# Performance work log

Measured on AMD Instinct MI355X. Metric: run time of the kernel, lower is better.

The kernel has to match this reference:

```python
import jax, jax.numpy as jnp
import numpy as np
from math import sqrt

HEADS = 16
D_MODEL = 1024
HEAD_DIM = D_MODEL // HEADS  # 64
B, SEQ = 2, 2048


def setup_inputs() -> dict:
    key = jax.random.key(0)
    ks = jax.random.split(key, 8)
    k = jax.random.normal(ks[0], (B, SEQ, D_MODEL), dtype=jnp.float32)
    q = jax.random.normal(ks[1], (B, SEQ, D_MODEL), dtype=jnp.float32)
    v = jax.random.normal(ks[2], (B, SEQ, D_MODEL), dtype=jnp.float32)
    # causal mask, broadcast over batch and heads; masked_fill where mask == 0
    mask = jnp.tril(jnp.ones((SEQ, SEQ), dtype=jnp.int32))[None, None, :, :]
    s = 1.0 / sqrt(HEAD_DIM)
    Wq = jax.random.normal(ks[3], (HEAD_DIM, HEAD_DIM), dtype=jnp.float32) * s
    Wk = jax.random.normal(ks[4], (HEAD_DIM, HEAD_DIM), dtype=jnp.float32) * s
    Wv = jax.random.normal(ks[5], (HEAD_DIM, HEAD_DIM), dtype=jnp.float32) * s
    Wo = jax.random.normal(ks[6], (D_MODEL, D_MODEL), dtype=jnp.float32) * (1.0 / sqrt(D_MODEL))
    bo = jax.random.normal(ks[7], (D_MODEL,), dtype=jnp.float32) * 0.01
    return {"key": k, "query": q, "value": v, "mask": mask,
            "Wq": Wq, "Wk": Wk, "Wv": Wv, "Wo": Wo, "bo": bo}


def reference(key, query, value, mask, Wq, Wk, Wv, Wo, bo):
    b, q_len, d = query.shape
    k_len = key.shape[1]
    hd = d // HEADS
    # reshape to [b, len, heads, head_dim]
    k = key.reshape(b, k_len, HEADS, hd)
    q = query.reshape(b, q_len, HEADS, hd)
    v = value.reshape(b, k_len, HEADS, hd)
    # per-head-dim Linear (weights shared across heads); torch Linear: y = x @ W.T
    k = jnp.einsum('bkhd,ed->bkhe', k, Wk)
    q = jnp.einsum('bqhd,ed->bqhe', q, Wq)
    v = jnp.einsum('bvhd,ed->bvhe', v, Wv)
    # full attention matrix [b, h, q, k]
    product = jnp.einsum('bqhd,bkhd->bhqk', q, k)
    # NOTE: original masks BEFORE scaling by 1/sqrt(head_dim)
    product = jnp.where(mask == 0, jnp.float32(-1e20), product)
    product = product / jnp.float32(sqrt(hd))
    score = jax.nn.softmax(product, axis=-1)
    out = jnp.einsum('bhqv,bvhd->bqhd', score, v).reshape(b, q_len, d)
    out = out @ Wo.T + bo
    return out
```

## Files before the change

### kernel.cpp

```cpp
#include <hip/hip_runtime.h>

typedef __bf16 bf16x8 __attribute__((ext_vector_type(8)));
typedef float  f32x4  __attribute__((ext_vector_type(4)));
typedef unsigned int uint32x4 __attribute__((ext_vector_type(4)));

#define MFMA16(a, b, c) __builtin_amdgcn_mfma_f32_16x16x32_bf16((a), (b), (c), 0, 0, 0)

constexpr int SEQ = 2048;
constexpr int DM  = 1024;
constexpr int NH  = 16;
constexpr int HD  = 64;
constexpr int BATCH = 2;


__device__ inline bf16x8 ld8_f32(const float* p) {
    f32x4 a = *(const f32x4*)p;
    f32x4 b = *(const f32x4*)(p + 4);
    bf16x8 r;
    r[0] = (__bf16)a[0]; r[1] = (__bf16)a[1]; r[2] = (__bf16)a[2]; r[3] = (__bf16)a[3];
    r[4] = (__bf16)b[0]; r[5] = (__bf16)b[1]; r[6] = (__bf16)b[2]; r[7] = (__bf16)b[3];
    return r;
}

__global__ __launch_bounds__(256)
void proj_kernel(const float* __restrict__ Xq, const float* __restrict__ Xk,
                 const float* __restrict__ Xv,
                 const float* __restrict__ Wq, const float* __restrict__ Wk,
                 const float* __restrict__ Wv,
                 __bf16* __restrict__ Qp, __bf16* __restrict__ Kp,
                 __bf16* __restrict__ Vp)
{
    const int tid  = threadIdx.x;
    const int w    = tid >> 6;
    const int lane = tid & 63;
    const int quad = lane >> 4;
    const int l16  = lane & 15;
    const int sblk = blockIdx.x;
    const int bh   = blockIdx.y;
    const int tz   = blockIdx.z;

    const float* X = (tz == 0) ? Xq : (tz == 1) ? Xk : Xv;
    const float* W = (tz == 0) ? Wq : (tz == 1) ? Wk : Wv;
    __bf16*      O = (tz == 0) ? Qp : (tz == 1) ? Kp : Vp;
    const float scale = (tz == 0) ? (0.125f * 1.44269504088896f) : 1.0f;

    const int b = bh >> 4, h = bh & 15;
    const int mrow = sblk * 64 + w * 16 + l16;

    const size_t xoff = (size_t)(b * SEQ + mrow) * DM + h * HD + quad * 8;
    bf16x8 a0 = ld8_f32(X + xoff);
    bf16x8 a1 = ld8_f32(X + xoff + 32);

    f32x4 acc[4];
    #pragma unroll
    for (int nt = 0; nt < 4; ++nt) {
        const size_t woff = (size_t)(nt * 16 + l16) * HD + quad * 8;
        bf16x8 b0 = ld8_f32(W + woff);
        bf16x8 b1 = ld8_f32(W + woff + 32);
        f32x4 c = {0.f, 0.f, 0.f, 0.f};
        c = MFMA16(a0, b0, c);
        c = MFMA16(a1, b1, c);
        acc[nt] = c;
    }

    __bf16* obase = O + (size_t)bh * SEQ * HD;
    #pragma unroll
    for (int nt = 0; nt < 4; ++nt) {
        #pragma unroll
        for (int r = 0; r < 4; ++r) {
            const int srow = sblk * 64 + w * 16 + quad * 4 + r;
            obase[(size_t)srow * HD + nt * 16 + l16] = (__bf16)(acc[nt][r] * scale);
        }
    }
}

__global__ __launch_bounds__(256, 2)
void attn_kernel(const __bf16* __restrict__ Qp, const __bf16* __restrict__ Kp,
                 const __bf16* __restrict__ Vp, __bf16* __restrict__ AO)
{
    __shared__ __align__(16) unsigned int K_lds[2][64 * 36];
    __shared__ __align__(16) unsigned int VT2[2][64 * 36];
    __shared__ __align__(16) __bf16 P_lds[4][16 * 72];

    const int tid  = threadIdx.x;
    const int w    = tid >> 6;
    const int lane = tid & 63;
    const int quad = lane >> 4;
    const int l16  = lane & 15;
    const int pr   = blockIdx.x;
    const int bh   = blockIdx.y;

    const __bf16* Qb = Qp + (size_t)bh * SEQ * HD;
    const __bf16* Kb = Kp + (size_t)bh * SEQ * HD;
    const __bf16* Vb = Vp + (size_t)bh * SEQ * HD;

    bf16x8 onesf;
    #pragma unroll
    for (int i = 0; i < 8; ++i) onesf[i] = (l16 == 0) ? (__bf16)1.0f : (__bf16)0.0f;

    const int krow = tid >> 3, kcol = tid & 7;
    const int jp = tid & 31, d0 = (tid >> 5) * 8;

    #pragma unroll
    for (int phase = 0; phase < 2; ++phase) {
        const int tile = (phase == 0) ? (31 - pr) : pr;
        const int q0   = tile * 64;
        const int nkc  = tile + 1;

        __syncthreads();

        const int mrow = q0 + w * 16 + l16;
        bf16x8 qa0 = *(const bf16x8*)(Qb + (size_t)mrow * HD + quad * 8);
        bf16x8 qa1 = *(const bf16x8*)(Qb + (size_t)mrow * HD + quad * 8 + 32);

        f32x4 accO[4];
        #pragma unroll
        for (int nt = 0; nt < 4; ++nt) { f32x4 z = {0.f,0.f,0.f,0.f}; accO[nt] = z; }
        f32x4 acc5 = {0.f, 0.f, 0.f, 0.f};

        uint32x4 kpre0 = *(const uint32x4*)(Kb + (size_t)krow * HD + kcol * 8);
        uint32x4 kpre1 = *(const uint32x4*)(Kb + (size_t)(krow + 32) * HD + kcol * 8);
        uint32x4 vlo   = *(const uint32x4*)(Vb + (size_t)(2 * jp) * HD + d0);
        uint32x4 vhi   = *(const uint32x4*)(Vb + (size_t)(2 * jp + 1) * HD + d0);

        for (int kc = 0; kc < nkc; ++kc) {
            const int buf = kc & 1;
            *(uint32x4*)&K_lds[buf][krow * 36 + kcol * 4]        = kpre0;
            *(uint32x4*)&K_lds[buf][(krow + 32) * 36 + kcol * 4] = kpre1;
            #pragma unroll
            for (int i2 = 0; i2 < 4; ++i2) {
                const unsigned int va = vlo[i2], vb = vhi[i2];
                VT2[buf][(d0 + 2 * i2    ) * 36 + jp] = (va & 0xffffu) | (vb << 16);
                VT2[buf][(d0 + 2 * i2 + 1) * 36 + jp] = (va >> 16) | (vb & 0xffff0000u);
            }
            __syncthreads();

            if (kc + 1 < nkc) {
                const size_t o = (size_t)(kc + 1) * 64;
                kpre0 = *(const uint32x4*)(Kb + (o + krow) * HD + kcol * 8);
                kpre1 = *(const uint32x4*)(Kb + (o + krow + 32) * HD + kcol * 8);
                vlo   = *(const uint32x4*)(Vb + (o + 2 * jp) * HD + d0);
                vhi   = *(const uint32x4*)(Vb + (o + 2 * jp + 1) * HD + d0);
            }

            f32x4 s[4];
            #pragma unroll
            for (int nt = 0; nt < 4; ++nt) {
                const unsigned int* kb = &K_lds[buf][(nt * 16 + l16) * 36 + quad * 4];
                bf16x8 kb0 = *(const bf16x8*)(kb);
                bf16x8 kb1 = *(const bf16x8*)(kb + 16);
                f32x4 c = {0.f, 0.f, 0.f, 0.f};
                c = MFMA16(qa0, kb0, c);
                c = MFMA16(qa1, kb1, c);
                s[nt] = c;
            }
            if (kc == tile) {
                #pragma unroll
                for (int nt = 0; nt < 4; ++nt) {
                    const int j = kc * 64 + nt * 16 + l16;
                    #pragma unroll
                    for (int r = 0; r < 4; ++r) {
                        const int qrow = q0 + w * 16 + quad * 4 + r;
                        if (j > qrow) s[nt][r] = -1e30f;
                    }
                }
            }
            #pragma unroll
            for (int nt = 0; nt < 4; ++nt) {
                #pragma unroll
                for (int r = 0; r < 4; ++r) {
                    P_lds[w][(quad * 4 + r) * 72 + nt * 16 + l16] =
                        (__bf16)exp2f(s[nt][r]);
                }
            }
            asm volatile("" ::: "memory");
            bf16x8 pa0 = *(const bf16x8*)&P_lds[w][l16 * 72 + quad * 8];
            bf16x8 pa1 = *(const bf16x8*)&P_lds[w][l16 * 72 + quad * 8 + 32];
            #pragma unroll
            for (int nt = 0; nt < 4; ++nt) {
                const unsigned int* vb2 = &VT2[buf][(nt * 16 + l16) * 36 + quad * 4];
                bf16x8 vb0 = *(const bf16x8*)(vb2);
                bf16x8 vb1 = *(const bf16x8*)(vb2 + 16);
                accO[nt] = MFMA16(pa0, vb0, accO[nt]);
                accO[nt] = MFMA16(pa1, vb1, accO[nt]);
            }
            acc5 = MFMA16(pa0, onesf, acc5);
            acc5 = MFMA16(pa1, onesf, acc5);
        }

        const int b = bh >> 4, h = bh & 15;
        float inv[4];
        #pragma unroll
        for (int r = 0; r < 4; ++r) {
            const float ls = __shfl(acc5[r], quad * 16, 64);
            inv[r] = 1.0f / ls;
        }
        #pragma unroll
        for (int nt = 0; nt < 4; ++nt) {
            #pragma unroll
            for (int r = 0; r < 4; ++r) {
                const int qrow = q0 + w * 16 + quad * 4 + r;
                AO[(size_t)(b * SEQ + qrow) * DM + h * HD + nt * 16 + l16] =
                    (__bf16)(accO[nt][r] * inv[r]);
            }
        }
    }
}

__global__ __launch_bounds__(256)
void wconv_kernel(const float* __restrict__ Wo, __bf16* __restrict__ Wb)
{
    const size_t i = ((size_t)blockIdx.x * 256 + threadIdx.x) * 8;
    *(bf16x8*)(Wb + i) = ld8_f32(Wo + i);
}

__global__ __launch_bounds__(256)
void ogemm_kernel(const __bf16* __restrict__ AO, const __bf16* __restrict__ Wb,
                  const float* __restrict__ bo, float* __restrict__ out)
{
    __shared__ __align__(16) unsigned int A_lds[2][64 * 36];
    __shared__ __align__(16) unsigned int B_lds[2][128 * 36];

    const int tid  = threadIdx.x;
    const int w    = tid >> 6;
    const int lane = tid & 63;
    const int quad = lane >> 4;
    const int l16  = lane & 15;
    const int m0   = blockIdx.x * 64;
    const int n0   = blockIdx.y * 128;

    const int row = tid >> 3, c = tid & 7;

    f32x4 acc[8];
    #pragma unroll
    for (int nt = 0; nt < 8; ++nt) { f32x4 z = {0.f,0.f,0.f,0.f}; acc[nt] = z; }

    uint32x4 apre[2], bpre[4];
    #pragma unroll
    for (int i = 0; i < 2; ++i)
        apre[i] = *(const uint32x4*)(AO + (size_t)(m0 + row + i * 32) * DM + c * 8);
    #pragma unroll
    for (int i = 0; i < 4; ++i)
        bpre[i] = *(const uint32x4*)(Wb + (size_t)(n0 + row + i * 32) * DM + c * 8);

    for (int kc = 0; kc < DM / 64; ++kc) {
        const int buf = kc & 1;
        #pragma unroll
        for (int i = 0; i < 2; ++i)
            *(uint32x4*)&A_lds[buf][(row + i * 32) * 36 + c * 4] = apre[i];
        #pragma unroll
        for (int i = 0; i < 4; ++i)
            *(uint32x4*)&B_lds[buf][(row + i * 32) * 36 + c * 4] = bpre[i];
        __syncthreads();

        if (kc + 1 < DM / 64) {
            const size_t o = (size_t)(kc + 1) * 64;
            #pragma unroll
            for (int i = 0; i < 2; ++i)
                apre[i] = *(const uint32x4*)(AO + (size_t)(m0 + row + i * 32) * DM + o + c * 8);
            #pragma unroll
            for (int i = 0; i < 4; ++i)
                bpre[i] = *(const uint32x4*)(Wb + (size_t)(n0 + row + i * 32) * DM + o + c * 8);
        }

        #pragma unroll
        for (int ks = 0; ks < 2; ++ks) {
            bf16x8 a = *(const bf16x8*)&A_lds[buf][(w * 16 + l16) * 36 + ks * 16 + quad * 4];
            #pragma unroll
            for (int nt = 0; nt < 8; ++nt) {
                bf16x8 bb = *(const bf16x8*)&B_lds[buf][(nt * 16 + l16) * 36 + ks * 16 + quad * 4];
                acc[nt] = MFMA16(a, bb, acc[nt]);
            }
        }
    }

    #pragma unroll
    for (int nt = 0; nt < 8; ++nt) {
        const int n = n0 + nt * 16 + l16;
        const float bof = bo[n];
        #pragma unroll
        for (int r = 0; r < 4; ++r) {
            const int m = m0 + w * 16 + quad * 4 + r;
            out[(size_t)m * DM + n] = acc[nt][r] + bof;
        }
    }
}

extern "C" void kernel_launch(void* const* d_in, const int* in_sizes, int n_in,
                              void* d_out, int out_size, void* d_ws, size_t ws_size,
                              hipStream_t stream)
{
    const float* key   = (const float*)d_in[0];
    const float* query = (const float*)d_in[1];
    const float* value = (const float*)d_in[2];
    const float* Wq = (const float*)d_in[4];
    const float* Wk = (const float*)d_in[5];
    const float* Wv = (const float*)d_in[6];
    const float* Wo = (const float*)d_in[7];
    const float* bo = (const float*)d_in[8];

    const size_t per = (size_t)BATCH * NH * SEQ * HD;
    __bf16* Qp = (__bf16*)d_ws;
    __bf16* Kp = Qp + per;
    __bf16* Vp = Kp + per;
    __bf16* AO = Vp + per;
    __bf16* Wb = Kp;

    proj_kernel<<<dim3(SEQ / 64, BATCH * NH, 3), 256, 0, stream>>>(
        query, key, value, Wq, Wk, Wv, Qp, Kp, Vp);
    attn_kernel<<<dim3(SEQ / 128, BATCH * NH), 256, 0, stream>>>(Qp, Kp, Vp, AO);
    wconv_kernel<<<dim3(DM * DM / (256 * 8)), 256, 0, stream>>>(Wo, Wb);
    ogemm_kernel<<<dim3(BATCH * SEQ / 64, DM / 128), 256, 0, stream>>>(
        AO, Wb, bo, (float*)d_out);
}
```

Before: 198.7 us.

## Keep softmax probabilities in registers via transposed S and 16x16x16 MFMA for PV

Result: no change. 200.1 us (+0.7%).

```diff
diff --git a/kernel.cpp b/kernel.cpp
--- a/kernel.cpp
+++ b/kernel.cpp
@@ -3,8 +3,10 @@
 typedef __bf16 bf16x8 __attribute__((ext_vector_type(8)));
 typedef float  f32x4  __attribute__((ext_vector_type(4)));
 typedef unsigned int uint32x4 __attribute__((ext_vector_type(4)));
-
-#define MFMA16(a, b, c) __builtin_amdgcn_mfma_f32_16x16x32_bf16((a), (b), (c), 0, 0, 0)
+typedef short  s16x4  __attribute__((ext_vector_type(4)));
+
+#define MFMA16(a, b, c)  __builtin_amdgcn_mfma_f32_16x16x32_bf16((a), (b), (c), 0, 0, 0)
+#define MFMAK16(a, b, c) __builtin_amdgcn_mfma_f32_16x16x16bf16_1k((a), (b), (c), 0, 0, 0)
 
 constexpr int SEQ = 2048;
 constexpr int DM  = 1024;
@@ -12,6 +14,8 @@
 constexpr int HD  = 64;
 constexpr int BATCH = 2;
 
+
+union Bf4 { __bf16 h[4]; s16x4 v; unsigned int u[2]; };
 
 __device__ inline bf16x8 ld8_f32(const float* p) {
     f32x4 a = *(const f32x4*)p;
@@ -80,7 +84,6 @@
 {
     __shared__ __align__(16) unsigned int K_lds[2][64 * 36];
     __shared__ __align__(16) unsigned int VT2[2][64 * 36];
-    __shared__ __align__(16) __bf16 P_lds[4][16 * 72];
 
     const int tid  = threadIdx.x;
     const int w    = tid >> 6;
@@ -94,9 +97,9 @@
     const __bf16* Kb = Kp + (size_t)bh * SEQ * HD;
     const __bf16* Vb = Vp + (size_t)bh * SEQ * HD;
 
-    bf16x8 onesf;
-    #pragma unroll
-    for (int i = 0; i < 8; ++i) onesf[i] = (l16 == 0) ? (__bf16)1.0f : (__bf16)0.0f;
+    Bf4 ones_a;
+    #pragma unroll
+    for (int i = 0; i < 4; ++i) ones_a.h[i] = (l16 == 0) ? (__bf16)1.0f : (__bf16)0.0f;
 
     const int krow = tid >> 3, kcol = tid & 7;
     const int jp = tid & 31, d0 = (tid >> 5) * 8;
@@ -109,13 +112,13 @@
 
         __syncthreads();
 
-        const int mrow = q0 + w * 16 + l16;
-        bf16x8 qa0 = *(const bf16x8*)(Qb + (size_t)mrow * HD + quad * 8);
-        bf16x8 qa1 = *(const bf16x8*)(Qb + (size_t)mrow * HD + quad * 8 + 32);
-
-        f32x4 accO[4];
-        #pragma unroll
-        for (int nt = 0; nt < 4; ++nt) { f32x4 z = {0.f,0.f,0.f,0.f}; accO[nt] = z; }
+        const int qrow = q0 + w * 16 + l16;
+        bf16x8 qa0 = *(const bf16x8*)(Qb + (size_t)qrow * HD + quad * 8);
+        bf16x8 qa1 = *(const bf16x8*)(Qb + (size_t)qrow * HD + quad * 8 + 32);
+
+        f32x4 accT[4];
+        #pragma unroll
+        for (int dm = 0; dm < 4; ++dm) { f32x4 z = {0.f,0.f,0.f,0.f}; accT[dm] = z; }
         f32x4 acc5 = {0.f, 0.f, 0.f, 0.f};
 
         uint32x4 kpre0 = *(const uint32x4*)(Kb + (size_t)krow * HD + kcol * 8);
@@ -143,66 +146,57 @@
                 vhi   = *(const uint32x4*)(Vb + (o + 2 * jp + 1) * HD + d0);
             }
 
-            f32x4 s[4];
+            f32x4 st[4];
             #pragma unroll
             for (int nt = 0; nt < 4; ++nt) {
                 const unsigned int* kb = &K_lds[buf][(nt * 16 + l16) * 36 + quad * 4];
                 bf16x8 kb0 = *(const bf16x8*)(kb);
                 bf16x8 kb1 = *(const bf16x8*)(kb + 16);
                 f32x4 c = {0.f, 0.f, 0.f, 0.f};
-                c = MFMA16(qa0, kb0, c);
-                c = MFMA16(qa1, kb1, c);
-                s[nt] = c;
+                c = MFMA16(kb0, qa0, c);
+                c = MFMA16(kb1, qa1, c);
+                st[nt] = c;
             }
             if (kc == tile) {
                 #pragma unroll
                 for (int nt = 0; nt < 4; ++nt) {
-                    const int j = kc * 64 + nt * 16 + l16;
                     #pragma unroll
                     for (int r = 0; r < 4; ++r) {
-                        const int qrow = q0 + w * 16 + quad * 4 + r;
-                        if (j > qrow) s[nt][r] = -1e30f;
+                        const int j = kc * 64 + nt * 16 + quad * 4 + r;
+                        if (j > qrow) st[nt][r] = -1e30f;
                     }
                 }
             }
+            Bf4 pf[4];
             #pragma unroll
             for (int nt = 0; nt < 4; ++nt) {
                 #pragma unroll
-                for (int r = 0; r < 4; ++r) {
-                    P_lds[w][(quad * 4 + r) * 72 + nt * 16 + l16] =
-                        (__bf16)exp2f(s[nt][r]);
+                for (int r = 0; r < 4; ++r) pf[nt].h[r] = (__bf16)exp2f(st[nt][r]);
+            }
+            #pragma unroll
+            for (int nt = 0; nt < 4; ++nt) {
+                #pragma unroll
+                for (int dm = 0; dm < 4; ++dm) {
+                    Bf4 va;
+                    va.u[0] = VT2[buf][(dm * 16 + l16) * 36 + nt * 8 + quad * 2];
+                    va.u[1] = VT2[buf][(dm * 16 + l16) * 36 + nt * 8 + quad * 2 + 1];
+                    accT[dm] = MFMAK16(va.v, pf[nt].v, accT[dm]);
                 }
-            }
-            asm volatile("" ::: "memory");
-            bf16x8 pa0 = *(const bf16x8*)&P_lds[w][l16 * 72 + quad * 8];
-            bf16x8 pa1 = *(const bf16x8*)&P_lds[w][l16 * 72 + quad * 8 + 32];
-            #pragma unroll
-            for (int nt = 0; nt < 4; ++nt) {
-                const unsigned int* vb2 = &VT2[buf][(nt * 16 + l16) * 36 + quad * 4];
-                bf16x8 vb0 = *(const bf16x8*)(vb2);
-                bf16x8 vb1 = *(const bf16x8*)(vb2 + 16);
-                accO[nt] = MFMA16(pa0, vb0, accO[nt]);
-                accO[nt] = MFMA16(pa1, vb1, accO[nt]);
-            }
-            acc5 = MFMA16(pa0, onesf, acc5);
-            acc5 = MFMA16(pa1, onesf, acc5);
+                acc5 = MFMAK16(ones_a.v, pf[nt].v, acc5);
+            }
         }
 
         const int b = bh >> 4, h = bh & 15;
-        float inv[4];
-        #pragma unroll
-        for (int r = 0; r < 4; ++r) {
-            const float ls = __shfl(acc5[r], quad * 16, 64);
-            inv[r] = 1.0f / ls;
-        }
-        #pragma unroll
-        for (int nt = 0; nt < 4; ++nt) {
-            #pragma unroll
-            for (int r = 0; r < 4; ++r) {
-                const int qrow = q0 + w * 16 + quad * 4 + r;
-                AO[(size_t)(b * SEQ + qrow) * DM + h * HD + nt * 16 + l16] =
-                    (__bf16)(accO[nt][r] * inv[r]);
-            }
+        const float ls  = __shfl(acc5[0], l16, 64);
+        const float inv = 1.0f / ls;
+        #pragma unroll
+        for (int dm = 0; dm < 4; ++dm) {
+            Bf4 ov;
+            #pragma unroll
+            for (int r = 0; r < 4; ++r) ov.h[r] = (__bf16)(accT[dm][r] * inv);
+            *(unsigned long long*)(AO + (size_t)(b * SEQ + qrow) * DM + h * HD
+                                   + dm * 16 + quad * 4) =
+                *(const unsigned long long*)&ov.u[0];
         }
     }
 }
```
